# Optimization experiments

Measured on AMD Instinct MI355X. Metric: run time of the kernel, lower is better.

The kernel has to match this reference:

```python
import jax, jax.numpy as jnp
import numpy as np

H, D, S, MID, S_OUT = 8, 1024, 1024, 2048, 512
EPS = 1e-6

def setup_inputs() -> dict:
    key = jax.random.key(0)
    ks = jax.random.split(key, 20)
    sc = 0.02
    inp = {
        'inp': jax.random.normal(ks[0], (D, S), jnp.float32),
        'enc_k': jax.random.normal(ks[1], (D, S), jnp.float32),
        'enc_v': jax.random.normal(ks[2], (D, S), jnp.float32),
        'w_qkv1': jax.random.normal(ks[3], (3, D, D), jnp.float32) * sc,
        'w_qkv2': jax.random.normal(ks[4], (3, D, D), jnp.float32) * sc,
        # per-head per-qkv MLPs: Linear(S->MID) then Linear(MID->S), torch layout [out,in]
        'mh1_W1': jax.random.normal(ks[5], (H, 3, MID, S), jnp.float32) * sc,
        'mh1_W2': jax.random.normal(ks[6], (H, 3, S, MID), jnp.float32) * sc,
        'mh2_W1': jax.random.normal(ks[7], (H, 3, MID, S), jnp.float32) * sc,
        'mh2_W2': jax.random.normal(ks[8], (H, 3, S, MID), jnp.float32) * sc,
        'c1_w1': jax.random.normal(ks[9], (MID, D * H), jnp.float32) * sc,
        'c1_w2': jax.random.normal(ks[10], (D, MID), jnp.float32) * sc,
        'c2_w1': jax.random.normal(ks[11], (MID, D * H), jnp.float32) * sc,
        'c2_w2': jax.random.normal(ks[12], (D, MID), jnp.float32) * sc,
        'l1_w1': jax.random.normal(ks[13], (MID, S), jnp.float32) * sc,
        'l1_w2': jax.random.normal(ks[14], (S_OUT, MID), jnp.float32) * sc,
        'l2_w1': jax.random.normal(ks[15], (MID, S_OUT), jnp.float32) * sc,
        'l2_w2': jax.random.normal(ks[16], (S_OUT, MID), jnp.float32) * sc,
        'gamma': jnp.ones((S,), jnp.float32),
        'beta': jnp.zeros((S,), jnp.float32),
    }
    return inp

def _layernorm(x, g, b):
    mu = jnp.mean(x, axis=-1, keepdims=True)
    var = jnp.var(x, axis=-1, keepdims=True)
    return (x - mu) / jnp.sqrt(var + EPS) * g + b

def _head_mlp(qkv, W1, W2):
    # qkv: [3, D, S]; W1: [H,3,MID,S]; W2: [H,3,S,MID]
    z = jnp.einsum('qds,hqms->hqdm', jax.nn.relu(qkv), W1)
    return jnp.einsum('hqdm,hqsm->hqds', jax.nn.relu(z), W2)  # [H,3,D,S]

def _mha_block(qkv, W1, W2, cw1, cw2):
    s = _head_mlp(qkv, W1, W2)
    q, k, v = s[:, 0], s[:, 1], s[:, 2]            # each [H,D,S]
    b = jnp.einsum('hdi,hdj->hij', k, q)            # k.T @ q per head (no softmax)
    att = jnp.einsum('hds,hst->hdt', v, b)          # [H,D,S]
    cat = att.reshape(H * D, -1)                    # concat over dim 0
    y = jnp.einsum('sc,mc->sm', jax.nn.relu(cat.T), cw1)
    y = jnp.einsum('sm,dm->sd', jax.nn.relu(y), cw2)
    return y.T                                      # [D,S]

def reference(inp, enc_k, enc_v, w_qkv1, w_qkv2, mh1_W1, mh1_W2, mh2_W1, mh2_W2,
              c1_w1, c1_w2, c2_w1, c2_w2, l1_w1, l1_w2, l2_w1, l2_w2, gamma, beta):
    # block 1: self-attention qkv
    qkv1 = jnp.einsum('qij,js->qis', w_qkv1, inp)   # [3,D,S]
    m1 = _mha_block(qkv1, mh1_W1, mh1_W2, c1_w1, c1_w2)
    h1 = _layernorm(inp + m1, gamma, beta)
    # block 2: q from h1, k/v from encoder
    q2 = jnp.matmul(w_qkv2[0], h1)
    qkv2 = jnp.stack([q2, enc_k, enc_v], axis=0)
    m2 = _mha_block(qkv2, mh2_W1, mh2_W2, c2_w1, c2_w2)
    h2 = _layernorm(inp + m2, gamma, beta)
    # output head
    x = jnp.einsum('ds,ms->dm', jax.nn.relu(h2), l1_w1)
    x = jnp.einsum('dm,om->do', jax.nn.relu(x), l1_w2)   # [D, S_OUT]
    y = jnp.einsum('do,mo->dm', jax.nn.relu(x), l2_w1)
    y = jnp.einsum('dm,om->do', jax.nn.relu(y), l2_w2)
    return jnp.tanh(y)
```

## Files before the change

### kernel.cpp

```cpp
#include <hip/hip_runtime.h>
#include <math.h>

#define H_    8
#define D_    1024
#define S_    1024
#define MID_  2048
#define SOUT_ 512
#define MAXB  24
#define LDP   72

typedef __bf16 bf16;
typedef __bf16 bf16x8 __attribute__((ext_vector_type(8)));
typedef float  floatx4 __attribute__((ext_vector_type(4)));

struct GemmArgs {
  const void* A[MAXB];
  const void* B[MAXB];
  void*       C[MAXB];
};

template <typename T>
__device__ __forceinline__ bf16x8 load8(const T* p);

template <>
__device__ __forceinline__ bf16x8 load8<float>(const float* p) {
  floatx4 a = *(const floatx4*)p;
  floatx4 b = *(const floatx4*)(p + 4);
  bf16x8 r;
  r[0] = (bf16)a[0]; r[1] = (bf16)a[1]; r[2] = (bf16)a[2]; r[3] = (bf16)a[3];
  r[4] = (bf16)b[0]; r[5] = (bf16)b[1]; r[6] = (bf16)b[2]; r[7] = (bf16)b[3];
  return r;
}
template <>
__device__ __forceinline__ bf16x8 load8<bf16>(const bf16* p) {
  return *(const bf16x8*)p;
}

template <typename TA, typename TB, typename TC>
__global__ __launch_bounds__(256, 2)
void gemm_bt_kernel(GemmArgs ga, int K, int ldc, int epi) {
  __shared__ __align__(16) bf16 As[128 * LDP];
  __shared__ __align__(16) bf16 Bs[128 * LDP];

  const TA* __restrict__ A = (const TA*)ga.A[blockIdx.z] + (size_t)blockIdx.y * 128 * K;
  const TB* __restrict__ B = (const TB*)ga.B[blockIdx.z] + (size_t)blockIdx.x * 128 * K;
  TC* __restrict__ C = (TC*)ga.C[blockIdx.z];

  const int t    = threadIdx.x;
  const int lane = t & 63;
  const int wave = t >> 6;
  const int wm   = (wave >> 1) * 64;
  const int wn   = (wave & 1) * 64;
  const int m16  = lane & 15;
  const int quad = lane >> 4;

  floatx4 acc[4][4];
#pragma unroll
  for (int i = 0; i < 4; i++)
#pragma unroll
    for (int j = 0; j < 4; j++) acc[i][j] = (floatx4){0.f, 0.f, 0.f, 0.f};

  for (int k0 = 0; k0 < K; k0 += 64) {
    bf16x8 sa[4], sb[4];
#pragma unroll
    for (int i = 0; i < 4; i++) {
      const int L   = i * 256 + t;
      const int row = L >> 3;
      const int c   = L & 7;
      const size_t goff = (size_t)row * K + k0 + c * 8;
      sa[i] = load8<TA>(A + goff);
      sb[i] = load8<TB>(B + goff);
    }
    __syncthreads();
#pragma unroll
    for (int i = 0; i < 4; i++) {
      const int L   = i * 256 + t;
      const int row = L >> 3;
      const int c   = L & 7;
      *(bf16x8*)&As[row * LDP + c * 8] = sa[i];
      *(bf16x8*)&Bs[row * LDP + c * 8] = sb[i];
    }
    __syncthreads();
#pragma unroll
    for (int ks = 0; ks < 2; ks++) {
      bf16x8 af[4], bfr[4];
#pragma unroll
      for (int f = 0; f < 4; f++) {
        const int ra = wm + f * 16 + m16;
        af[f]  = *(const bf16x8*)&As[ra * LDP + (ks * 4 + quad) * 8];
        const int rb = wn + f * 16 + m16;
        bfr[f] = *(const bf16x8*)&Bs[rb * LDP + (ks * 4 + quad) * 8];
      }
#pragma unroll
      for (int fi = 0; fi < 4; fi++)
#pragma unroll
        for (int fj = 0; fj < 4; fj++)
          acc[fi][fj] = __builtin_amdgcn_mfma_f32_16x16x32_bf16(af[fi], bfr[fj], acc[fi][fj], 0, 0, 0);
    }
  }

  const size_t cm0 = (size_t)blockIdx.y * 128 + wm + quad * 4;
  const size_t cn0 = (size_t)blockIdx.x * 128 + wn + m16;
#pragma unroll
  for (int fi = 0; fi < 4; fi++)
#pragma unroll
    for (int fj = 0; fj < 4; fj++)
#pragma unroll
      for (int r = 0; r < 4; r++) {
        float v = acc[fi][fj][r];
        if (epi == 1) v = fmaxf(v, 0.f);
        else if (epi == 2) v = tanhf(v);
        C[(cm0 + fi * 16 + r) * (size_t)ldc + cn0 + fj * 16] = (TC)v;
      }
}

__global__ void transpose_kernel(const float* __restrict__ in, bf16* __restrict__ out,
                                 int R, int Cc) {
  __shared__ bf16 tile[32][33];
  const int bx = blockIdx.x * 32, by = blockIdx.y * 32;
  const int tx = threadIdx.x, ty = threadIdx.y;
#pragma unroll
  for (int i = 0; i < 32; i += 8) tile[ty + i][tx] = (bf16)in[(size_t)(by + ty + i) * Cc + bx + tx];
  __syncthreads();
#pragma unroll
  for (int i = 0; i < 32; i += 8) out[(size_t)(bx + ty + i) * R + by + tx] = tile[tx][ty + i];
}

__global__ void relu_copy_kernel(const float* __restrict__ in, bf16* __restrict__ out, int n) {
  int i = blockIdx.x * 256 + threadIdx.x;
  if (i < n) out[i] = (bf16)fmaxf(in[i], 0.f);
}

__global__ void add_ln_kernel(const float* __restrict__ inp, const bf16* __restrict__ yT,
                              const float* __restrict__ gamma, const float* __restrict__ beta,
                              bf16* __restrict__ out, int transpose_out) {
  const int d = blockIdx.x;
  const int t = threadIdx.x;
  __shared__ float sh1[8], sh2[8];
  float vals[4], sum = 0.f, sq = 0.f;
#pragma unroll
  for (int i = 0; i < 4; i++) {
    const int s = t + i * 256;
    float v = inp[(size_t)d * 1024 + s] + (float)yT[(size_t)s * 1024 + d];
    vals[i] = v; sum += v; sq += v * v;
  }
  for (int off = 32; off > 0; off >>= 1) { sum += __shfl_down(sum, off); sq += __shfl_down(sq, off); }
  const int wave = t >> 6, lane = t & 63;
  if (lane == 0) { sh1[wave] = sum; sh2[wave] = sq; }
  __syncthreads();
  if (t == 0) {
    float s1 = sh1[0] + sh1[1] + sh1[2] + sh1[3];
    float s2 = sh2[0] + sh2[1] + sh2[2] + sh2[3];
    sh1[4] = s1 * (1.f / 1024.f);
    sh2[4] = s2 * (1.f / 1024.f);
  }
  __syncthreads();
  const float mu  = sh1[4];
  const float var = fmaxf(sh2[4] - mu * mu, 0.f);
  const float rs  = rsqrtf(var + 1e-6f);
#pragma unroll
  for (int i = 0; i < 4; i++) {
    const int s = t + i * 256;
    float nv = (vals[i] - mu) * rs * gamma[s] + beta[s];
    if (transpose_out) out[(size_t)s * 1024 + d] = (bf16)nv;
    else               out[(size_t)d * 1024 + s] = (bf16)fmaxf(nv, 0.f);
  }
}

static inline void gemm_launch(hipStream_t st, const GemmArgs& ga, int nb,
                               int M, int N, int K, int ldc, int epi,
                               bool a32, bool b32, bool c32) {
  dim3 grid(N / 128, M / 128, nb), blk(256);
  if      ( a32 && !b32 && !c32) gemm_bt_kernel<float, bf16, bf16><<<grid, blk, 0, st>>>(ga, K, ldc, epi);
  else if (!a32 &&  b32 && !c32) gemm_bt_kernel<bf16, float, bf16><<<grid, blk, 0, st>>>(ga, K, ldc, epi);
  else if (!a32 &&  b32 &&  c32) gemm_bt_kernel<bf16, float, float><<<grid, blk, 0, st>>>(ga, K, ldc, epi);
  else                           gemm_bt_kernel<bf16, bf16, bf16><<<grid, blk, 0, st>>>(ga, K, ldc, epi);
}

static void run_block(hipStream_t st, int CH,
                      const bf16* qkv0, const bf16* qkv1p, const bf16* qkv2p,
                      const float* W1, const float* W2,
                      const float* cw1, const float* cw2,
                      bf16* rcatT, bf16* chunk) {
  const size_t M1 = (size_t)1024 * 1024;
  bf16* rz  = chunk;
  bf16* qkT = chunk + (size_t)CH * 6 * M1;
  bf16* vb  = chunk + (size_t)CH * 8 * M1;
  bf16* bT  = chunk + (size_t)CH * 9 * M1;
  const bf16* qkvp[3] = {qkv0, qkv1p, qkv2p};

  for (int h0 = 0; h0 < H_; h0 += CH) {
    GemmArgs ga{};
    for (int b = 0; b < 3 * CH; b++) {
      const int h = h0 + b / 3, q = b % 3;
      ga.A[b] = qkvp[q];
      ga.B[b] = W1 + (size_t)(h * 3 + q) * MID_ * S_;
      ga.C[b] = rz + (size_t)b * D_ * MID_;
    }
    gemm_launch(st, ga, 3 * CH, D_, MID_, S_, MID_, 1, false, true, false);
    for (int b = 0; b < 2 * CH; b++) {
      const int hh = b / 2, q = b % 2;
      ga.A[b] = W2 + (size_t)((h0 + hh) * 3 + q) * S_ * MID_;
      ga.B[b] = rz + (size_t)(hh * 3 + q) * D_ * MID_;
      ga.C[b] = qkT + (size_t)b * S_ * D_;
    }
    gemm_launch(st, ga, 2 * CH, S_, D_, MID_, D_, 0, true, false, false);
    for (int b = 0; b < CH; b++) {
      ga.A[b] = rz + (size_t)(b * 3 + 2) * D_ * MID_;
      ga.B[b] = W2 + (size_t)((h0 + b) * 3 + 2) * S_ * MID_;
      ga.C[b] = vb + (size_t)b * D_ * S_;
    }
    gemm_launch(st, ga, CH, D_, S_, MID_, S_, 0, false, true, false);
    for (int b = 0; b < CH; b++) {
      ga.A[b] = qkT + (size_t)(b * 2 + 0) * S_ * D_;
      ga.B[b] = qkT + (size_t)(b * 2 + 1) * S_ * D_;
      ga.C[b] = bT + (size_t)b * S_ * S_;
    }
    gemm_launch(st, ga, CH, S_, S_, D_, S_, 0, false, false, false);
    for (int b = 0; b < CH; b++) {
      ga.A[b] = bT + (size_t)b * S_ * S_;
      ga.B[b] = vb + (size_t)b * D_ * S_;
      ga.C[b] = rcatT + (size_t)(h0 + b) * D_;
    }
    gemm_launch(st, ga, CH, S_, D_, S_, H_ * D_, 1, false, false, false);
  }
  bf16* ry1 = chunk;
  bf16* y2  = chunk + 2 * M1;
  GemmArgs ga{};
  ga.A[0] = rcatT; ga.B[0] = cw1; ga.C[0] = ry1;
  gemm_launch(st, ga, 1, S_, MID_, H_ * D_, MID_, 1, false, true, false);
  ga.A[0] = ry1; ga.B[0] = cw2; ga.C[0] = y2;
  gemm_launch(st, ga, 1, S_, D_, MID_, D_, 0, false, true, false);
}

extern "C" void kernel_launch(void* const* d_in, const int* in_sizes, int n_in,
                              void* d_out, int out_size, void* d_ws, size_t ws_size,
                              hipStream_t stream) {
  (void)in_sizes; (void)n_in; (void)out_size;
  const float* inp    = (const float*)d_in[0];
  const float* enc_k  = (const float*)d_in[1];
  const float* enc_v  = (const float*)d_in[2];
  const float* w_qkv1 = (const float*)d_in[3];
  const float* w_qkv2 = (const float*)d_in[4];
  const float* mh1_W1 = (const float*)d_in[5];
  const float* mh1_W2 = (const float*)d_in[6];
  const float* mh2_W1 = (const float*)d_in[7];
  const float* mh2_W2 = (const float*)d_in[8];
  const float* c1_w1  = (const float*)d_in[9];
  const float* c1_w2  = (const float*)d_in[10];
  const float* c2_w1  = (const float*)d_in[11];
  const float* c2_w2  = (const float*)d_in[12];
  const float* l1_w1  = (const float*)d_in[13];
  const float* l1_w2  = (const float*)d_in[14];
  const float* l2_w1  = (const float*)d_in[15];
  const float* l2_w2  = (const float*)d_in[16];
  const float* gamma  = (const float*)d_in[17];
  const float* beta   = (const float*)d_in[18];
  float* out = (float*)d_out;
  bf16*  ws  = (bf16*)d_ws;

  const size_t M1 = (size_t)1024 * 1024;
  bf16* inpT  = ws;
  bf16* rqkv  = ws + 1 * M1;
  bf16* rcatT = ws + 4 * M1;
  bf16* h1T   = ws + 12 * M1;
  bf16* rh2   = ws + 13 * M1;
  bf16* renck = ws + 14 * M1;
  bf16* rencv = ws + 15 * M1;
  bf16* chunk = ws + 16 * M1;

  const size_t avail = ws_size / sizeof(bf16);
  int CH = 1;
  if      (16 * M1 + 80 * M1 <= avail) CH = 8;
  else if (16 * M1 + 40 * M1 <= avail) CH = 4;
  else if (16 * M1 + 20 * M1 <= avail) CH = 2;

  transpose_kernel<<<dim3(S_ / 32, D_ / 32), dim3(32, 8), 0, stream>>>(inp, inpT, D_, S_);

  {
    GemmArgs ga{};
    ga.A[0] = w_qkv1; ga.B[0] = inpT; ga.C[0] = rqkv;
    gemm_launch(stream, ga, 1, 3 * D_, S_, D_, S_, 1, true, false, false);
  }

  run_block(stream, CH, rqkv, rqkv + M1, rqkv + 2 * M1, mh1_W1, mh1_W2, c1_w1, c1_w2, rcatT, chunk);
  bf16* y2 = chunk + 2 * M1;
  add_ln_kernel<<<dim3(D_), dim3(256), 0, stream>>>(inp, y2, gamma, beta, h1T, 1);

  relu_copy_kernel<<<dim3(4096), dim3(256), 0, stream>>>(enc_k, renck, (int)M1);
  relu_copy_kernel<<<dim3(4096), dim3(256), 0, stream>>>(enc_v, rencv, (int)M1);

  {
    GemmArgs ga{};
    ga.A[0] = w_qkv2; ga.B[0] = h1T; ga.C[0] = rqkv;
    gemm_launch(stream, ga, 1, D_, S_, D_, S_, 1, true, false, false);
  }

  run_block(stream, CH, rqkv, renck, rencv, mh2_W1, mh2_W2, c2_w1, c2_w2, rcatT, chunk);
  add_ln_kernel<<<dim3(D_), dim3(256), 0, stream>>>(inp, y2, gamma, beta, rh2, 0);

  bf16* rx1 = chunk;
  bf16* rx2 = chunk + 2 * M1;
  bf16* ryf = chunk + 3 * M1;
  {
    GemmArgs ga{};
    ga.A[0] = rh2; ga.B[0] = l1_w1; ga.C[0] = rx1;
    gemm_launch(stream, ga, 1, D_, MID_, S_, MID_, 1, false, true, false);
    ga.A[0] = rx1; ga.B[0] = l1_w2; ga.C[0] = rx2;
    gemm_launch(stream, ga, 1, D_, SOUT_, MID_, SOUT_, 1, false, true, false);
    ga.A[0] = rx2; ga.B[0] = l2_w1; ga.C[0] = ryf;
    gemm_launch(stream, ga, 1, D_, MID_, SOUT_, MID_, 1, false, true, false);
    ga.A[0] = ryf; ga.B[0] = l2_w2; ga.C[0] = out;
    gemm_launch(stream, ga, 1, D_, SOUT_, MID_, SOUT_, 2, false, true, true);
  }
}
```

Baseline: 2.305 ms.

## Pre-convert weights to bf16 and use direct global-to-LDS loads in GEMM

Result: no change. 2.351 ms (+2.0%).

```diff
diff --git a/kernel.cpp b/kernel.cpp
--- a/kernel.cpp
+++ b/kernel.cpp
@@ -36,14 +36,21 @@
   return *(const bf16x8*)p;
 }
 
-template <typename TA, typename TB, typename TC>
-__global__ __launch_bounds__(256, 2)
-void gemm_bt_kernel(GemmArgs ga, int K, int ldc, int epi) {
-  __shared__ __align__(16) bf16 As[128 * LDP];
-  __shared__ __align__(16) bf16 Bs[128 * LDP];
-
-  const TA* __restrict__ A = (const TA*)ga.A[blockIdx.z] + (size_t)blockIdx.y * 128 * K;
-  const TB* __restrict__ B = (const TB*)ga.B[blockIdx.z] + (size_t)blockIdx.x * 128 * K;
+__device__ __forceinline__ void gload16(const void* g, void* l) {
+  __builtin_amdgcn_global_load_lds(
+      (const __attribute__((address_space(1))) void*)g,
+      (__attribute__((address_space(3))) void*)l,
+      16, 0, 0);
+}
+
+template <typename TC>
+__global__ __launch_bounds__(256, 3)
+void gemm_lds_kernel(GemmArgs ga, int K, int ldc, int epi) {
+  __shared__ __align__(16) bf16 As[128 * 64];
+  __shared__ __align__(16) bf16 Bs[128 * 64];
+
+  const bf16* __restrict__ A = (const bf16*)ga.A[blockIdx.z] + (size_t)blockIdx.y * 128 * K;
+  const bf16* __restrict__ B = (const bf16*)ga.B[blockIdx.z] + (size_t)blockIdx.x * 128 * K;
   TC* __restrict__ C = (TC*)ga.C[blockIdx.z];
 
   const int t    = threadIdx.x;
@@ -54,6 +61,87 @@
   const int m16  = lane & 15;
   const int quad = lane >> 4;
 
+  size_t goff[4];
+  int    loff[4];
+#pragma unroll
+  for (int i = 0; i < 4; i++) {
+    const int Lb  = (i * 4 + wave) * 64;
+    const int row = (Lb >> 3) + (lane >> 3);
+    const int c   = lane & 7;
+    goff[i] = (size_t)row * K + (size_t)c * 8;
+    loff[i] = Lb * 8;
+  }
+
+  floatx4 acc[4][4];
+#pragma unroll
+  for (int i = 0; i < 4; i++)
+#pragma unroll
+    for (int j = 0; j < 4; j++) acc[i][j] = (floatx4){0.f, 0.f, 0.f, 0.f};
+
+  for (int k0 = 0; k0 < K; k0 += 64) {
+    __syncthreads();
+#pragma unroll
+    for (int i = 0; i < 4; i++) {
+      gload16(A + goff[i] + k0, &As[loff[i]]);
+      gload16(B + goff[i] + k0, &Bs[loff[i]]);
+    }
+    __syncthreads();
+#pragma unroll
+    for (int ks = 0; ks < 2; ks++) {
+      bf16x8 af[4], bfr[4];
+#pragma unroll
+      for (int f = 0; f < 4; f++) {
+        af[f]  = *(const bf16x8*)&As[(wm + f * 16 + m16) * 64 + (ks * 4 + quad) * 8];
+        bfr[f] = *(const bf16x8*)&Bs[(wn + f * 16 + m16) * 64 + (ks * 4 + quad) * 8];
+      }
+#pragma unroll
+      for (int fi = 0; fi < 4; fi++)
+#pragma unroll
+        for (int fj = 0; fj < 4; fj++)
+          acc[fi][fj] = __builtin_amdgcn_mfma_f32_16x16x32_bf16(af[fi], bfr[fj], acc[fi][fj], 0, 0, 0);
+    }
+  }
+
+  const size_t cm0 = (size_t)blockIdx.y * 128 + wm + quad * 4;
+  const size_t cn0 = (size_t)blockIdx.x * 128 + wn + m16;
+#pragma unroll
+  for (int fi = 0; fi < 4; fi++)
+#pragma unroll
+    for (int fj = 0; fj < 4; fj++)
+#pragma unroll
+      for (int r = 0; r < 4; r++) {
+        float v = acc[fi][fj][r];
+        if (epi == 1) v = fmaxf(v, 0.f);
+        else if (epi == 2) v = tanhf(v);
+        C[(cm0 + fi * 16 + r) * (size_t)ldc + cn0 + fj * 16] = (TC)v;
+      }
+}
+
+static inline void gemm_lds_launch(hipStream_t st, const GemmArgs& ga, int nb,
+                                   int M, int N, int K, int ldc, int epi, bool c32) {
+  dim3 grid(N / 128, M / 128, nb), blk(256);
+  if (c32) gemm_lds_kernel<float><<<grid, blk, 0, st>>>(ga, K, ldc, epi);
+  else     gemm_lds_kernel<bf16 ><<<grid, blk, 0, st>>>(ga, K, ldc, epi);
+}
+
+template <typename TA, typename TB, typename TC>
+__global__ __launch_bounds__(256, 2)
+void gemm_bt_kernel(GemmArgs ga, int K, int ldc, int epi) {
+  __shared__ __align__(16) bf16 As[128 * LDP];
+  __shared__ __align__(16) bf16 Bs[128 * LDP];
+
+  const TA* __restrict__ A = (const TA*)ga.A[blockIdx.z] + (size_t)blockIdx.y * 128 * K;
+  const TB* __restrict__ B = (const TB*)ga.B[blockIdx.z] + (size_t)blockIdx.x * 128 * K;
+  TC* __restrict__ C = (TC*)ga.C[blockIdx.z];
+
+  const int t    = threadIdx.x;
+  const int lane = t & 63;
+  const int wave = t >> 6;
+  const int wm   = (wave >> 1) * 64;
+  const int wn   = (wave & 1) * 64;
+  const int m16  = lane & 15;
+  const int quad = lane >> 4;
+
   floatx4 acc[4][4];
 #pragma unroll
   for (int i = 0; i < 4; i++)
@@ -114,6 +202,16 @@
       }
 }
 
+static inline void gemm_launch_f32(hipStream_t st, const GemmArgs& ga, int nb,
+                                   int M, int N, int K, int ldc, int epi,
+                                   bool a32, bool b32, bool c32) {
+  dim3 grid(N / 128, M / 128, nb), blk(256);
+  if      ( a32 && !b32 && !c32) gemm_bt_kernel<float, bf16, bf16><<<grid, blk, 0, st>>>(ga, K, ldc, epi);
+  else if (!a32 &&  b32 && !c32) gemm_bt_kernel<bf16, float, bf16><<<grid, blk, 0, st>>>(ga, K, ldc, epi);
+  else if (!a32 &&  b32 &&  c32) gemm_bt_kernel<bf16, float, float><<<grid, blk, 0, st>>>(ga, K, ldc, epi);
+  else                           gemm_bt_kernel<bf16, bf16, bf16><<<grid, blk, 0, st>>>(ga, K, ldc, epi);
+}
+
 __global__ void transpose_kernel(const float* __restrict__ in, bf16* __restrict__ out,
                                  int R, int Cc) {
   __shared__ bf16 tile[32][33];
@@ -129,6 +227,15 @@
 __global__ void relu_copy_kernel(const float* __restrict__ in, bf16* __restrict__ out, int n) {
   int i = blockIdx.x * 256 + threadIdx.x;
   if (i < n) out[i] = (bf16)fmaxf(in[i], 0.f);
+}
+
+__global__ void cvt32to16_kernel(const float* __restrict__ in, bf16* __restrict__ out, size_t n) {
+  size_t i = ((size_t)blockIdx.x * 256 + threadIdx.x) * 8;
+  if (i + 8 <= n) *(bf16x8*)&out[i] = load8<float>(&in[i]);
+}
+
+static inline void cvt(hipStream_t st, const float* src, bf16* dst, size_t n) {
+  cvt32to16_kernel<<<dim3((unsigned)(n / 2048)), dim3(256), 0, st>>>(src, dst, n);
 }
 
 __global__ void add_ln_kernel(const float* __restrict__ inp, const bf16* __restrict__ yT,
@@ -167,21 +274,11 @@
   }
 }
 
-static inline void gemm_launch(hipStream_t st, const GemmArgs& ga, int nb,
-                               int M, int N, int K, int ldc, int epi,
-                               bool a32, bool b32, bool c32) {
-  dim3 grid(N / 128, M / 128, nb), blk(256);
-  if      ( a32 && !b32 && !c32) gemm_bt_kernel<float, bf16, bf16><<<grid, blk, 0, st>>>(ga, K, ldc, epi);
-  else if (!a32 &&  b32 && !c32) gemm_bt_kernel<bf16, float, bf16><<<grid, blk, 0, st>>>(ga, K, ldc, epi);
-  else if (!a32 &&  b32 &&  c32) gemm_bt_kernel<bf16, float, float><<<grid, blk, 0, st>>>(ga, K, ldc, epi);
-  else                           gemm_bt_kernel<bf16, bf16, bf16><<<grid, blk, 0, st>>>(ga, K, ldc, epi);
-}
-
-static void run_block(hipStream_t st, int CH,
-                      const bf16* qkv0, const bf16* qkv1p, const bf16* qkv2p,
-                      const float* W1, const float* W2,
-                      const float* cw1, const float* cw2,
-                      bf16* rcatT, bf16* chunk) {
+static void run_block_lds(hipStream_t st, int CH,
+                          const bf16* qkv0, const bf16* qkv1p, const bf16* qkv2p,
+                          const bf16* W1, const bf16* W2,
+                          const bf16* cw1, const bf16* cw2,
+                          bf16* rcatT, bf16* chunk) {
   const size_t M1 = (size_t)1024 * 1024;
   bf16* rz  = chunk;
   bf16* qkT = chunk + (size_t)CH * 6 * M1;
@@ -197,40 +294,96 @@
       ga.B[b] = W1 + (size_t)(h * 3 + q) * MID_ * S_;
       ga.C[b] = rz + (size_t)b * D_ * MID_;
     }
-    gemm_launch(st, ga, 3 * CH, D_, MID_, S_, MID_, 1, false, true, false);
+    gemm_lds_launch(st, ga, 3 * CH, D_, MID_, S_, MID_, 1, false);
     for (int b = 0; b < 2 * CH; b++) {
       const int hh = b / 2, q = b % 2;
       ga.A[b] = W2 + (size_t)((h0 + hh) * 3 + q) * S_ * MID_;
       ga.B[b] = rz + (size_t)(hh * 3 + q) * D_ * MID_;
       ga.C[b] = qkT + (size_t)b * S_ * D_;
     }
-    gemm_launch(st, ga, 2 * CH, S_, D_, MID_, D_, 0, true, false, false);
+    gemm_lds_launch(st, ga, 2 * CH, S_, D_, MID_, D_, 0, false);
     for (int b = 0; b < CH; b++) {
       ga.A[b] = rz + (size_t)(b * 3 + 2) * D_ * MID_;
       ga.B[b] = W2 + (size_t)((h0 + b) * 3 + 2) * S_ * MID_;
       ga.C[b] = vb + (size_t)b * D_ * S_;
     }
-    gemm_launch(st, ga, CH, D_, S_, MID_, S_, 0, false, true, false);
+    gemm_lds_launch(st, ga, CH, D_, S_, MID_, S_, 0, false);
     for (int b = 0; b < CH; b++) {
       ga.A[b] = qkT + (size_t)(b * 2 + 0) * S_ * D_;
       ga.B[b] = qkT + (size_t)(b * 2 + 1) * S_ * D_;
       ga.C[b] = bT + (size_t)b * S_ * S_;
     }
-    gemm_launch(st, ga, CH, S_, S_, D_, S_, 0, false, false, false);
+    gemm_lds_launch(st, ga, CH, S_, S_, D_, S_, 0, false);
     for (int b = 0; b < CH; b++) {
       ga.A[b] = bT + (size_t)b * S_ * S_;
       ga.B[b] = vb + (size_t)b * D_ * S_;
       ga.C[b] = rcatT + (size_t)(h0 + b) * D_;
     }
-    gemm_launch(st, ga, CH, S_, D_, S_, H_ * D_, 1, false, false, false);
+    gemm_lds_launch(st, ga, CH, S_, D_, S_, H_ * D_, 1, false);
   }
   bf16* ry1 = chunk;
   bf16* y2  = chunk + 2 * M1;
   GemmArgs ga{};
   ga.A[0] = rcatT; ga.B[0] = cw1; ga.C[0] = ry1;
-  gemm_launch(st, ga, 1, S_, MID_, H_ * D_, MID_, 1, false, true, false);
+  gemm_lds_launch(st, ga, 1, S_, MID_, H_ * D_, MID_, 1, false);
   ga.A[0] = ry1; ga.B[0] = cw2; ga.C[0] = y2;
-  gemm_launch(st, ga, 1, S_, D_, MID_, D_, 0, false, true, false);
+  gemm_lds_launch(st, ga, 1, S_, D_, MID_, D_, 0, false);
+}
+
+static void run_block_f32(hipStream_t st, int CH,
+                          const bf16* qkv0, const bf16* qkv1p, const bf16* qkv2p,
+                          const float* W1, const float* W2,
+                          const float* cw1, const float* cw2,
+                          bf16* rcatT, bf16* chunk) {
+  const size_t M1 = (size_t)1024 * 1024;
+  bf16* rz  = chunk;
+  bf16* qkT = chunk + (size_t)CH * 6 * M1;
+  bf16* vb  = chunk + (size_t)CH * 8 * M1;
+  bf16* bT  = chunk + (size_t)CH * 9 * M1;
+  const bf16* qkvp[3] = {qkv0, qkv1p, qkv2p};
+
+  for (int h0 = 0; h0 < H_; h0 += CH) {
+    GemmArgs ga{};
+    for (int b = 0; b < 3 * CH; b++) {
+      const int h = h0 + b / 3, q = b % 3;
+      ga.A[b] = qkvp[q];
+      ga.B[b] = W1 + (size_t)(h * 3 + q) * MID_ * S_;
+      ga.C[b] = rz + (size_t)b * D_ * MID_;
+    }
+    gemm_launch_f32(st, ga, 3 * CH, D_, MID_, S_, MID_, 1, false, true, false);
+    for (int b = 0; b < 2 * CH; b++) {
+      const int hh = b / 2, q = b % 2;
+      ga.A[b] = W2 + (size_t)((h0 + hh) * 3 + q) * S_ * MID_;
+      ga.B[b] = rz + (size_t)(hh * 3 + q) * D_ * MID_;
+      ga.C[b] = qkT + (size_t)b * S_ * D_;
+    }
+    gemm_launch_f32(st, ga, 2 * CH, S_, D_, MID_, D_, 0, true, false, false);
+    for (int b = 0; b < CH; b++) {
+      ga.A[b] = rz + (size_t)(b * 3 + 2) * D_ * MID_;
+      ga.B[b] = W2 + (size_t)((h0 + b) * 3 + 2) * S_ * MID_;
+      ga.C[b] = vb + (size_t)b * D_ * S_;
+    }
+    gemm_launch_f32(st, ga, CH, D_, S_, MID_, S_, 0, false, true, false);
+    for (int b = 0; b < CH; b++) {
+      ga.A[b] = qkT + (size_t)(b * 2 + 0) * S_ * D_;
+      ga.B[b] = qkT + (size_t)(b * 2 + 1) * S_ * D_;
+      ga.C[b] = bT + (size_t)b * S_ * S_;
+    }
+    gemm_launch_f32(st, ga, CH, S_, S_, D_, S_, 0, false, false, false);
+    for (int b = 0; b < CH; b++) {
+      ga.A[b] = bT + (size_t)b * S_ * S_;
+      ga.B[b] = vb + (size_t)b * D_ * S_;
+      ga.C[b] = rcatT + (size_t)(h0 + b) * D_;
+    }
+    gemm_launch_f32(st, ga, CH, S_, D_, S_, H_ * D_, 1, false, false, false);
+  }
+  bf16* ry1 = chunk;
+  bf16* y2  = chunk + 2 * M1;
+  GemmArgs ga{};
+  ga.A[0] = rcatT; ga.B[0] = cw1; ga.C[0] = ry1;
+  gemm_launch_f32(st, ga, 1, S_, MID_, H_ * D_, MID_, 1, false, true, false);
+  ga.A[0] = ry1; ga.B[0] = cw2; ga.C[0] = y2;
+  gemm_launch_f32(st, ga, 1, S_, D_, MID_, D_, 0, false, true, false);
 }
 
 extern "C" void kernel_launch(void* const* d_in, const int* in_sizes, int n_in,
@@ -260,6 +413,16 @@
   bf16*  ws  = (bf16*)d_ws;
 
   const size_t M1 = (size_t)1024 * 1024;
+  const size_t avail = ws_size / sizeof(bf16);
+
+  int  CH   = 0;
+  bool dual = false;
+  if      (avail >= (29 + 224 + 80) * M1) { CH = 8; dual = true; }
+  else if (avail >= (29 + 112 + 80) * M1) CH = 8;
+  else if (avail >= (29 + 112 + 40) * M1) CH = 4;
+  else if (avail >= (29 + 112 + 20) * M1) CH = 2;
+  else if (avail >= (29 + 112 + 10) * M1) CH = 1;
+
   bf16* inpT  = ws;
   bf16* rqkv  = ws + 1 * M1;
   bf16* rcatT = ws + 4 * M1;
@@ -267,36 +430,114 @@
   bf16* rh2   = ws + 13 * M1;
   bf16* renck = ws + 14 * M1;
   bf16* rencv = ws + 15 * M1;
-  bf16* chunk = ws + 16 * M1;
-
-  const size_t avail = ws_size / sizeof(bf16);
-  int CH = 1;
-  if      (16 * M1 + 80 * M1 <= avail) CH = 8;
-  else if (16 * M1 + 40 * M1 <= avail) CH = 4;
-  else if (16 * M1 + 20 * M1 <= avail) CH = 2;
+
+  if (CH == 0) {
+    bf16* chunk = ws + 16 * M1;
+    int CHo = 1;
+    if      (16 * M1 + 80 * M1 <= avail) CHo = 8;
+    else if (16 * M1 + 40 * M1 <= avail) CHo = 4;
+    else if (16 * M1 + 20 * M1 <= avail) CHo = 2;
+
+    transpose_kernel<<<dim3(S_ / 32, D_ / 32), dim3(32, 8), 0, stream>>>(inp, inpT, D_, S_);
+    {
+      GemmArgs ga{};
+      ga.A[0] = w_qkv1; ga.B[0] = inpT; ga.C[0] = rqkv;
+      gemm_launch_f32(stream, ga, 1, 3 * D_, S_, D_, S_, 1, true, false, false);
+    }
+    run_block_f32(stream, CHo, rqkv, rqkv + M1, rqkv + 2 * M1, mh1_W1, mh1_W2, c1_w1, c1_w2, rcatT, chunk);
+    bf16* y2 = chunk + 2 * M1;
+    add_ln_kernel<<<dim3(D_), dim3(256), 0, stream>>>(inp, y2, gamma, beta, h1T, 1);
+    relu_copy_kernel<<<dim3(4096), dim3(256), 0, stream>>>(enc_k, renck, (int)M1);
+    relu_copy_kernel<<<dim3(4096), dim3(256), 0, stream>>>(enc_v, rencv, (int)M1);
+    {
+      GemmArgs ga{};
+      ga.A[0] = w_qkv2; ga.B[0] = h1T; ga.C[0] = rqkv;
+      gemm_launch_f32(stream, ga, 1, D_, S_, D_, S_, 1, true, false, false);
+    }
+    run_block_f32(stream, CHo, rqkv, renck, rencv, mh2_W1, mh2_W2, c2_w1, c2_w2, rcatT, chunk);
+    add_ln_kernel<<<dim3(D_), dim3(256), 0, stream>>>(inp, y2, gamma, beta, rh2, 0);
+    bf16* rx1 = chunk;
+    bf16* rx2 = chunk + 2 * M1;
+    bf16* ryf = chunk + 3 * M1;
+    {
+      GemmArgs ga{};
+      ga.A[0] = rh2; ga.B[0] = l1_w1; ga.C[0] = rx1;
+      gemm_launch_f32(stream, ga, 1, D_, MID_, S_, MID_, 1, false, true, false);
+      ga.A[0] = rx1; ga.B[0] = l1_w2; ga.C[0] = rx2;
+      gemm_launch_f32(stream, ga, 1, D_, SOUT_, MID_, SOUT_, 1, false, true, false);
+      ga.A[0] = rx2; ga.B[0] = l2_w1; ga.C[0] = ryf;
+      gemm_launch_f32(stream, ga, 1, D_, MID_, SOUT_, MID_, 1, false, true, false);
+      ga.A[0] = ryf; ga.B[0] = l2_w2; ga.C[0] = out;
+      gemm_launch_f32(stream, ga, 1, D_, SOUT_, MID_, SOUT_, 2, false, true, true);
+    }
+    return;
+  }
+
+  bf16* wqkv1b = ws + 16 * M1;
+  bf16* wq2b   = ws + 19 * M1;
+  bf16* c1w2b  = ws + 20 * M1;
+  bf16* c2w2b  = ws + 22 * M1;
+  bf16* l1w1b  = ws + 24 * M1;
+  bf16* l1w2b  = ws + 26 * M1;
+  bf16* l2w1b  = ws + 27 * M1;
+  bf16* l2w2b  = ws + 28 * M1;
+  bf16* wblkA  = ws + 29 * M1;
+  bf16* wblkB  = dual ? wblkA + 112 * M1 : wblkA;
+  bf16* chunk  = ws + (29 + (dual ? 224 : 112)) * M1;
+
+  bf16* W1bA  = wblkA;
+  bf16* W2bA  = wblkA + 48 * M1;
+  bf16* cw1bA = wblkA + 96 * M1;
+  bf16* W1bB  = wblkB;
+  bf16* W2bB  = wblkB + 48 * M1;
+  bf16* cw1bB = wblkB + 96 * M1;
+
+  const size_t NW  = (size_t)H_ * 3 * MID_ * S_;
+  const size_t NC1 = (size_t)MID_ * H_ * D_;
 
   transpose_kernel<<<dim3(S_ / 32, D_ / 32), dim3(32, 8), 0, stream>>>(inp, inpT, D_, S_);
+  cvt(stream, w_qkv1, wqkv1b, (size_t)3 * M1);
+  cvt(stream, w_qkv2, wq2b, M1);
+  cvt(stream, c1_w2, c1w2b, (size_t)2 * M1);
+  cvt(stream, c2_w2, c2w2b, (size_t)2 * M1);
+  cvt(stream, l1_w1, l1w1b, (size_t)2 * M1);
+  cvt(stream, l1_w2, l1w2b, M1);
+  cvt(stream, l2_w1, l2w1b, M1);
+  cvt(stream, l2_w2, l2w2b, M1);
+  cvt(stream, mh1_W1, W1bA, NW);
+  cvt(stream, mh1_W2, W2bA, NW);
+  cvt(stream, c1_w1, cw1bA, NC1);
+  if (dual) {
+    cvt(stream, mh2_W1, W1bB, NW);
+    cvt(stream, mh2_W2, W2bB, NW);
+    cvt(stream, c2_w1, cw1bB, NC1);
+  }
+  relu_copy_kernel<<<dim3(4096), dim3(256), 0, stream>>>(enc_k, renck, (int)M1);
+  relu_copy_kernel<<<dim3(4096), dim3(256), 0, stream>>>(enc_v, rencv, (int)M1);
 
   {
     GemmArgs ga{};
-    ga.A[0] = w_qkv1; ga.B[0] = inpT; ga.C[0] = rqkv;
-    gemm_launch(stream, ga, 1, 3 * D_, S_, D_, S_, 1, true, false, false);
-  }
-
-  run_block(stream, CH, rqkv, rqkv + M1, rqkv + 2 * M1, mh1_W1, mh1_W2, c1_w1, c1_w2, rcatT, chunk);
+    ga.A[0] = wqkv1b; ga.B[0] = inpT; ga.C[0] = rqkv;
+    gemm_lds_launch(stream, ga, 1, 3 * D_, S_, D_, S_, 1, false);
+  }
+
+  run_block_lds(stream, CH, rqkv, rqkv + M1, rqkv + 2 * M1, W1bA, W2bA, cw1bA, c1w2b, rcatT, chunk);
   bf16* y2 = chunk + 2 * M1;
   add_ln_kernel<<<dim3(D_), dim3(256), 0, stream>>>(inp, y2, gamma, beta, h1T, 1);
 
-  relu_copy_kernel<<<dim3(4096), dim3(256), 0, stream>>>(enc_k, renck, (int)M1);
-  relu_copy_kernel<<<dim3(4096), dim3(256), 0, stream>>>(enc_v, rencv, (int)M1);
+  if (!dual) {
+    cvt(stream, mh2_W1, W1bB, NW);
+    cvt(stream, mh2_W2, W2bB, NW);
+    cvt(stream, c2_w1, cw1bB, NC1);
+  }
 
   {
     GemmArgs ga{};
-    ga.A[0] = w_qkv2; ga.B[0] = h1T; ga.C[0] = rqkv;
-    gemm_launch(stream, ga, 1, D_, S_, D_, S_, 1, true, false, false);
-  }
-
-  run_block(stream, CH, rqkv, renck, rencv, mh2_W1, mh2_W2, c2_w1, c2_w2, rcatT, chunk);
+    ga.A[0] = wq2b; ga.B[0] = h1T; ga.C[0] = rqkv;
+    gemm_lds_launch(stream, ga, 1, D_, S_, D_, S_, 1, false);
+  }
+
+  run_block_lds(stream, CH, rqkv, renck, rencv, W1bB, W2bB, cw1bB, c2w2b, rcatT, chunk);
   add_ln_kernel<<<dim3(D_), dim3(256), 0, stream>>>(inp, y2, gamma, beta, rh2, 0);
 
   bf16* rx1 = chunk;
@@ -304,13 +545,13 @@
   bf16* ryf = chunk + 3 * M1;
   {
     GemmArgs ga{};
-    ga.A[0] = rh2; ga.B[0] = l1_w1; ga.C[0] = rx1;
-    gemm_launch(stream, ga, 1, D_, MID_, S_, MID_, 1, false, true, false);
-    ga.A[0] = rx1; ga.B[0] = l1_w2; ga.C[0] = rx2;
-    gemm_launch(stream, ga, 1, D_, SOUT_, MID_, SOUT_, 1, false, true, false);
-    ga.A[0] = rx2; ga.B[0] = l2_w1; ga.C[0] = ryf;
-    gemm_launch(stream, ga, 1, D_, MID_, SOUT_, MID_, 1, false, true, false);
-    ga.A[0] = ryf; ga.B[0] = l2_w2; ga.C[0] = out;
-    gemm_launch(stream, ga, 1, D_, SOUT_, MID_, SOUT_, 2, false, true, true);
-  }
-}
+    ga.A[0] = rh2; ga.B[0] = l1w1b; ga.C[0] = rx1;
+    gemm_lds_launch(stream, ga, 1, D_, MID_, S_, MID_, 1, false);
+    ga.A[0] = rx1; ga.B[0] = l1w2b; ga.C[0] = rx2;
+    gemm_lds_launch(stream, ga, 1, D_, SOUT_, MID_, SOUT_, 1, false);
+    ga.A[0] = rx2; ga.B[0] = l2w1b; ga.C[0] = ryf;
+    gemm_lds_launch(stream, ga, 1, D_, MID_, SOUT_, MID_, 1, false);
+    ga.A[0] = ryf; ga.B[0] = l2w2b; ga.C[0] = out;
+    gemm_lds_launch(stream, ga, 1, D_, SOUT_, MID_, SOUT_, 2, true);
+  }
+}
```
